# Performance work log

Measured on AMD Instinct MI355X. Metric: run time of the kernel, lower is better.

Reference implementation:

```python
import jax, jax.numpy as jnp
import numpy as np

K, N = 4, 128
NODEDIM = 256
EDGEDIM_IN = 256
EDGEDIM_OUT = 256
GLOBALDIM = 256
INFODIM = 2 * NODEDIM + GLOBALDIM + EDGEDIM_IN  # 1024


def setup_inputs() -> dict:
    key = jax.random.key(0)
    ks = jax.random.split(key, 10)
    u = jax.random.normal(ks[0], (K, GLOBALDIM), dtype=jnp.float32)
    h_v = jax.random.normal(ks[1], (K, N, NODEDIM), dtype=jnp.float32)
    h_e = jax.random.normal(ks[2], (K, N, N, EDGEDIM_IN), dtype=jnp.float32)
    V = jax.random.randint(ks[3], (K, N), 0, 2).astype(jnp.float32)  # binary node mask
    E = jax.random.randint(ks[4], (K, N, N, 2), 0, 2, dtype=jnp.int32)  # per-type edge mask
    # function[1] params (loop runs i in [1, num_functions) -> only i=1)
    s1 = 1.0 / np.sqrt(INFODIM)
    W1 = jax.random.uniform(ks[5], (INFODIM, INFODIM), jnp.float32, -s1, s1)
    b1 = jax.random.uniform(ks[6], (INFODIM,), jnp.float32, -s1, s1)
    W2 = jax.random.uniform(ks[7], (INFODIM, EDGEDIM_OUT), jnp.float32, -s1, s1)
    b2 = jax.random.uniform(ks[8], (EDGEDIM_OUT,), jnp.float32, -s1, s1)
    return {"u": u, "h_v": h_v, "h_e": h_e, "V": V, "E": E,
            "W1": W1, "b1": b1, "W2": W2, "b2": b2}


def reference(u, h_v, h_e, V, E, W1, b1, W2, b2):
    Kb, Nn = h_v.shape[0], h_v.shape[1]
    hv = h_v * V[..., None]                                    # masked node states
    src = jnp.broadcast_to(hv[:, :, None, :], (Kb, Nn, Nn, NODEDIM))
    tgt = jnp.broadcast_to(hv[:, None, :, :], (Kb, Nn, Nn, NODEDIM))
    glb = jnp.broadcast_to(u[:, None, None, :], (Kb, Nn, Nn, GLOBALDIM))
    edge_feat = jnp.concatenate([src, tgt, glb, h_e], axis=-1)  # [K,N,N,INFODIM]
    # per-type MLP (only function index 1 executes for num_functions=2)
    h = jax.nn.elu(jnp.einsum('knmi,ij->knmj', edge_feat, W1) + b1)
    out = jnp.einsum('knmi,io->knmo', h, W2) + b2               # [K,N,N,EDGEDIM_OUT]
    mask = (E[..., 1] == 1)[..., None]
    h_e_update = jnp.where(mask, out, jnp.zeros((), out.dtype))
    # residual=True, history=True
    return h_e_update + h_e
```

## Files before the change

kernel.cpp:

```cpp
#include <hip/hip_runtime.h>
#include <stdint.h>

#define DEVI __device__ __forceinline__

typedef short bf16x8 __attribute__((ext_vector_type(8)));
typedef float f32x4  __attribute__((ext_vector_type(4)));

DEVI short f2bf(float f){
  union { float f; uint32_t u; } un; un.f = f;
  uint32_t u = un.u;
  u += 0x7fffu + ((u >> 16) & 1u);
  return (short)(u >> 16);
}
DEVI float bf2f(uint32_t us){
  union { uint32_t u; float f; } x; x.u = us << 16; return x.f;
}

DEVI f32x4 mfma16(bf16x8 a, bf16x8 b, f32x4 c){
  return __builtin_amdgcn_mfma_f32_16x16x32_bf16(a, b, c, 0, 0, 0);
}

__global__ void transpose_bf(const float* __restrict__ W, short* __restrict__ WT,
                             int R, int C){
  __shared__ float tile[32][33];
  int ctiles = C >> 5;
  int bi = blockIdx.x / ctiles, bj = blockIdx.x % ctiles;
  int tx = threadIdx.x & 31, ty = threadIdx.x >> 5;
  #pragma unroll
  for (int r = 0; r < 4; ++r){
    int i = bi*32 + ty + r*8;
    tile[ty + r*8][tx] = W[(size_t)i*C + bj*32 + tx];
  }
  __syncthreads();
  #pragma unroll
  for (int r = 0; r < 4; ++r){
    int j = bj*32 + ty + r*8;
    WT[(size_t)j*R + bi*32 + tx] = f2bf(tile[tx][ty + r*8]);
  }
}

__global__ void prep_hv(const float* __restrict__ hv, const float* __restrict__ V,
                        const float* __restrict__ u, short* __restrict__ hvb,
                        short* __restrict__ ub){
  int idx = blockIdx.x*256 + threadIdx.x;
  if (idx < 512*256){
    int r = idx >> 8;
    hvb[idx] = f2bf(hv[idx] * V[r]);
  } else if (idx < 512*256 + 1024){
    int i2 = idx - 512*256;
    ub[i2] = f2bf(u[i2]);
  }
}

__global__ __launch_bounds__(256) void prep_st(
    const short* __restrict__ hvb, const short* __restrict__ ub,
    const short* __restrict__ w1t, const float* __restrict__ b1,
    short* __restrict__ sbuf, short* __restrict__ tbuf)
{
  const int bid = blockIdx.x;
  const int st = bid >> 7;
  const int rt8 = (bid >> 4) & 7;
  const int ctile = bid & 15;
  const int r0 = rt8 << 6, j0 = ctile << 6;
  const int tid = threadIdx.x;
  const int w = tid >> 6, l = tid & 63;
  const int l15 = l & 15, l4 = l >> 4;
  __shared__ short A[64*256];
  for (int q = 0; q < 8; ++q){
    int id = tid + (q << 8);
    int row = id >> 5, c8 = id & 31;
    bf16x8 v = *(const bf16x8*)(hvb + (size_t)(r0 + row)*256 + c8*8);
    *(bf16x8*)((char*)A + row*512 + ((c8*16) ^ ((row & 7) << 4))) = v;
  }
  __syncthreads();
  const int wr = w >> 1, wc = w & 1;
  const int rowbase = wr << 5, colbase = wc << 5;
  const int swzA = (l15 & 7) << 4;
  f32x4 acc[2][2];
  acc[0][0]=0; acc[0][1]=0; acc[1][0]=0; acc[1][1]=0;
  const int ioff = st ? 256 : 0;
  const short* w1p = w1t + (size_t)(j0 + colbase + l15)*1024 + ioff + l4*8;
  const char* ap0 = (const char*)A + (rowbase + l15)*512;
  const char* ap1 = ap0 + 16*512;
  #pragma unroll
  for (int kk = 0; kk < 8; ++kk){
    int ib = kk*64 + l4*16;
    bf16x8 a0 = *(const bf16x8*)(ap0 + (ib ^ swzA));
    bf16x8 a1 = *(const bf16x8*)(ap1 + (ib ^ swzA));
    bf16x8 b0 = *(const bf16x8*)(w1p + kk*32);
    bf16x8 b1v = *(const bf16x8*)(w1p + 16*1024 + kk*32);
    acc[0][0] = mfma16(a0, b0, acc[0][0]);
    acc[1][0] = mfma16(a1, b0, acc[1][0]);
    acc[0][1] = mfma16(a0, b1v, acc[0][1]);
    acc[1][1] = mfma16(a1, b1v, acc[1][1]);
  }
  if (st == 0){
    const int kb = r0 >> 7;
    const short* up = ub + kb*256 + l4*8;
    const short* w1pu = w1t + (size_t)(j0 + colbase + l15)*1024 + 512 + l4*8;
    #pragma unroll
    for (int kk = 0; kk < 8; ++kk){
      bf16x8 au = *(const bf16x8*)(up + kk*32);
      bf16x8 b0 = *(const bf16x8*)(w1pu + kk*32);
      bf16x8 b1v = *(const bf16x8*)(w1pu + 16*1024 + kk*32);
      acc[0][0] = mfma16(au, b0, acc[0][0]);
      acc[1][0] = mfma16(au, b0, acc[1][0]);
      acc[0][1] = mfma16(au, b1v, acc[0][1]);
      acc[1][1] = mfma16(au, b1v, acc[1][1]);
    }
  }
  #pragma unroll
  for (int r = 0; r < 2; ++r){
    #pragma unroll
    for (int c = 0; c < 2; ++c){
      int jg = j0 + colbase + c*16 + l15;
      float badd = st ? 0.f : b1[jg];
      #pragma unroll
      for (int reg = 0; reg < 4; ++reg){
        int rowl = rowbase + r*16 + l4*4 + reg;
        if (st == 0)
          sbuf[(size_t)(r0 + rowl)*1024 + jg] = f2bf(acc[r][c][reg] + badd);
        else
          tbuf[(size_t)jg*512 + (r0 + rowl)] = f2bf(acc[r][c][reg]);
      }
    }
  }
}

__global__ __launch_bounds__(256, 3) void fused_edge(
    const float* __restrict__ he, const unsigned short* __restrict__ sb,
    const unsigned short* __restrict__ tbT, const short* __restrict__ w1t,
    const short* __restrict__ w2t, const float* __restrict__ b2,
    const int* __restrict__ Em, float* __restrict__ out)
{
  const int b = blockIdx.x;
  const int k = b >> 8;
  const int n = (b >> 1) & 127;
  const int m0 = (b & 1) << 6;
  const int tid = threadIdx.x;
  const int w = tid >> 6, l = tid & 63;
  const int l15 = l & 15, l4 = l >> 4;

  __shared__ short heb[64*256];
  __shared__ short eluv[2][64*64];

  const int grow0 = ((k << 7) + n)*128 + m0;
  const float* hesrc = he + (size_t)grow0 * 256;

  #pragma unroll
  for (int q = 0; q < 8; ++q){
    int id = tid + (q << 8);
    int row = id >> 5, c8 = id & 31;
    const float4* p = (const float4*)(hesrc + row*256 + c8*8);
    float4 a4 = p[0], b4 = p[1];
    union { bf16x8 v; short s[8]; } pk;
    pk.s[0]=f2bf(a4.x); pk.s[1]=f2bf(a4.y); pk.s[2]=f2bf(a4.z); pk.s[3]=f2bf(a4.w);
    pk.s[4]=f2bf(b4.x); pk.s[5]=f2bf(b4.y); pk.s[6]=f2bf(b4.z); pk.s[7]=f2bf(b4.w);
    *(bf16x8*)((char*)heb + row*512 + ((c8*16) ^ ((row & 7) << 4))) = pk.v;
  }
  __syncthreads();

  f32x4 acc2[4][4];
  #pragma unroll
  for (int i = 0; i < 4; ++i)
    #pragma unroll
    for (int j = 0; j < 4; ++j) acc2[i][j] = 0;

  const unsigned short* srow = sb  + (size_t)((k << 7) + n)*1024;
  const unsigned short* tcol = tbT + (size_t)((k << 7) + m0);
  const char* hb = (const char*)heb;
  const int swz = (l15 & 7) << 4;

  union u4 { ushort4 v; unsigned short s[4]; };

  bf16x8 bw1[8];
  {
    const short* w1p = w1t + (size_t)(w*16 + l15)*1024 + 768 + l4*8;
    #pragma unroll
    for (int kk = 0; kk < 8; ++kk) bw1[kk] = *(const bf16x8*)(w1p + kk*32);
  }
  u4 t4[4];
  #pragma unroll
  for (int rt = 0; rt < 4; ++rt)
    t4[rt].v = *(const ushort4*)(tcol + (size_t)(w*16 + l15)*512 + rt*16 + l4*4);
  float sv = bf2f(srow[w*16 + l15]);

  #pragma unroll
  for (int jc = 0; jc < 16; ++jc){
    const int jcol = jc*64 + w*16 + l15;

    f32x4 acc1[4];
    acc1[0]=0; acc1[1]=0; acc1[2]=0; acc1[3]=0;
    #pragma unroll
    for (int kk = 0; kk < 8; ++kk){
      int ib = kk*64 + l4*16;
      #pragma unroll
      for (int rt = 0; rt < 4; ++rt){
        int row = rt*16 + l15;
        bf16x8 a = *(const bf16x8*)(hb + row*512 + (ib ^ swz));
        acc1[rt] = mfma16(a, bw1[kk], acc1[rt]);
      }
    }

    const short* w2p = w2t + (size_t)(w*64 + l15)*1024 + jc*64 + l4*8;
    bf16x8 bw2a[4];
    #pragma unroll
    for (int q = 0; q < 4; ++q)
      bw2a[q] = *(const bf16x8*)(w2p + (size_t)q*16*1024);

    if (jc < 15){
      const short* w1p = w1t + (size_t)(jcol + 64)*1024 + 768 + l4*8;
      #pragma unroll
      for (int kk = 0; kk < 8; ++kk) bw1[kk] = *(const bf16x8*)(w1p + kk*32);
    }

    char* eb = (char*)eluv[jc & 1];
    #pragma unroll
    for (int rt = 0; rt < 4; ++rt){
      #pragma unroll
      for (int reg = 0; reg < 4; ++reg){
        int row = rt*16 + l4*4 + reg;
        float v = acc1[rt][reg] + sv + bf2f(t4[rt].s[reg]);
        v = v > 0.f ? v : (__expf(v) - 1.f);
        *(short*)(eb + row*128 + ((((w*16 + l15)*2)) ^ ((row & 7) << 4))) = f2bf(v);
      }
    }

    if (jc < 15){
      #pragma unroll
      for (int rt = 0; rt < 4; ++rt)
        t4[rt].v = *(const ushort4*)(tcol + (size_t)(jcol + 64)*512 + rt*16 + l4*4);
      sv = bf2f(srow[jcol + 64]);
    }
    __syncthreads();

    bf16x8 bw2b[4];
    #pragma unroll
    for (int q = 0; q < 4; ++q)
      bw2b[q] = *(const bf16x8*)(w2p + (size_t)q*16*1024 + 32);

    {
      int jb = l4*16;
      #pragma unroll
      for (int rt = 0; rt < 4; ++rt){
        int row = rt*16 + l15;
        bf16x8 a2 = *(const bf16x8*)(eb + row*128 + (jb ^ swz));
        #pragma unroll
        for (int q = 0; q < 4; ++q)
          acc2[rt][q] = mfma16(a2, bw2a[q], acc2[rt][q]);
      }
      jb = 64 + l4*16;
      #pragma unroll
      for (int rt = 0; rt < 4; ++rt){
        int row = rt*16 + l15;
        bf16x8 a2 = *(const bf16x8*)(eb + row*128 + (jb ^ swz));
        #pragma unroll
        for (int q = 0; q < 4; ++q)
          acc2[rt][q] = mfma16(a2, bw2b[q], acc2[rt][q]);
      }
    }
  }

  float bias[4];
  #pragma unroll
  for (int q = 0; q < 4; ++q) bias[q] = b2[w*64 + q*16 + l15];
  #pragma unroll
  for (int rt = 0; rt < 4; ++rt){
    #pragma unroll
    for (int reg = 0; reg < 4; ++reg){
      int row = rt*16 + l4*4 + reg;
      size_t grow = (size_t)(grow0 + row);
      int2 ep = *(const int2*)(Em + grow*2);
      const float* hep = he + grow*256 + w*64 + l15;
      float* op = out + grow*256 + w*64 + l15;
      #pragma unroll
      for (int q = 0; q < 4; ++q){
        float v = (ep.y == 1) ? (acc2[rt][q][reg] + bias[q]) : 0.f;
        op[q*16] = v + hep[q*16];
      }
    }
  }
}

extern "C" void kernel_launch(void* const* d_in, const int* in_sizes, int n_in,
                              void* d_out, int out_size, void* d_ws, size_t ws_size,
                              hipStream_t stream)
{
  const float* u   = (const float*)d_in[0];
  const float* h_v = (const float*)d_in[1];
  const float* h_e = (const float*)d_in[2];
  const float* V   = (const float*)d_in[3];
  const int*   E   = (const int*)d_in[4];
  const float* W1  = (const float*)d_in[5];
  const float* b1  = (const float*)d_in[6];
  const float* W2  = (const float*)d_in[7];
  const float* b2  = (const float*)d_in[8];
  float* out = (float*)d_out;

  char* ws = (char*)d_ws;
  short* w1t  = (short*)(ws);
  short* w2t  = (short*)(ws + (2u<<20));
  short* hvb  = (short*)(ws + (2u<<20) + (512u<<10));
  short* ub   = (short*)(ws + (2u<<20) + (768u<<10));
  short* sbuf = (short*)(ws + (3u<<20));
  short* tbuf = (short*)(ws + (4u<<20));

  transpose_bf<<<1024, 256, 0, stream>>>(W1, w1t, 1024, 1024);
  transpose_bf<<<256,  256, 0, stream>>>(W2, w2t, 1024, 256);
  prep_hv<<<516, 256, 0, stream>>>(h_v, V, u, hvb, ub);
  prep_st<<<256, 256, 0, stream>>>(hvb, ub, w1t, b1, sbuf, tbuf);
  fused_edge<<<1024, 256, 0, stream>>>(h_e,
                                       (const unsigned short*)sbuf,
                                       (const unsigned short*)tbuf,
                                       w1t, w2t, b2, E, out);
}
```

Measured before the change: 201.8 us.

## Single-buffer ELU tile for higher occupancy, coalesce prep stores, nontemporal he traffic

The fused kernel drops the double-buffered ELU LDS tile in favour of one buffer with an extra barrier per column chunk. This cuts LDS per block so launch bounds can rise from 3 to 4 blocks per SIMD. The prep kernel now stages its output tile in shared memory and writes 16-byte coalesced rows instead of scattered 2-byte stores. h_e loads and output stores use nontemporal hints to avoid polluting cache. The extra barrier serialises the ELU write against the previous chunk's second GEMM, and the tighter launch bound may force register spills.

```diff
diff --git a/kernel.cpp b/kernel.cpp
--- a/kernel.cpp
+++ b/kernel.cpp
@@ -66,6 +66,7 @@
   const int w = tid >> 6, l = tid & 63;
   const int l15 = l & 15, l4 = l >> 4;
   __shared__ short A[64*256];
+  __shared__ short Stile[64][64];
   for (int q = 0; q < 8; ++q){
     int id = tid + (q << 8);
     int row = id >> 5, c8 = id & 31;
@@ -113,21 +114,31 @@
   for (int r = 0; r < 2; ++r){
     #pragma unroll
     for (int c = 0; c < 2; ++c){
-      int jg = j0 + colbase + c*16 + l15;
-      float badd = st ? 0.f : b1[jg];
+      int jl = colbase + c*16 + l15;
+      float badd = st ? 0.f : b1[j0 + jl];
       #pragma unroll
       for (int reg = 0; reg < 4; ++reg){
         int rowl = rowbase + r*16 + l4*4 + reg;
-        if (st == 0)
-          sbuf[(size_t)(r0 + rowl)*1024 + jg] = f2bf(acc[r][c][reg] + badd);
-        else
-          tbuf[(size_t)jg*512 + (r0 + rowl)] = f2bf(acc[r][c][reg]);
-      }
-    }
-  }
-}
-
-__global__ __launch_bounds__(256, 3) void fused_edge(
+        short v = f2bf(acc[r][c][reg] + badd);
+        if (st == 0) Stile[rowl][jl] = v;
+        else         Stile[jl][rowl] = v;
+      }
+    }
+  }
+  __syncthreads();
+  {
+    int a = tid >> 2, ch = (tid & 3) << 4;
+    bf16x8 v0 = *(const bf16x8*)(&Stile[a][ch]);
+    bf16x8 v1 = *(const bf16x8*)(&Stile[a][ch + 8]);
+    short* dst = (st == 0)
+      ? (sbuf + (size_t)(r0 + a)*1024 + j0 + ch)
+      : (tbuf + (size_t)(j0 + a)*512  + r0 + ch);
+    *(bf16x8*)(dst)     = v0;
+    *(bf16x8*)(dst + 8) = v1;
+  }
+}
+
+__global__ __launch_bounds__(256, 4) void fused_edge(
     const float* __restrict__ he, const unsigned short* __restrict__ sb,
     const unsigned short* __restrict__ tbT, const short* __restrict__ w1t,
     const short* __restrict__ w2t, const float* __restrict__ b2,
@@ -142,7 +153,7 @@
   const int l15 = l & 15, l4 = l >> 4;
 
   __shared__ short heb[64*256];
-  __shared__ short eluv[2][64*64];
+  __shared__ short eluv[64*64];
 
   const int grow0 = ((k << 7) + n)*128 + m0;
   const float* hesrc = he + (size_t)grow0 * 256;
@@ -151,8 +162,9 @@
   for (int q = 0; q < 8; ++q){
     int id = tid + (q << 8);
     int row = id >> 5, c8 = id & 31;
-    const float4* p = (const float4*)(hesrc + row*256 + c8*8);
-    float4 a4 = p[0], b4 = p[1];
+    const f32x4* p = (const f32x4*)(hesrc + row*256 + c8*8);
+    f32x4 a4 = __builtin_nontemporal_load(p);
+    f32x4 b4 = __builtin_nontemporal_load(p + 1);
     union { bf16x8 v; short s[8]; } pk;
     pk.s[0]=f2bf(a4.x); pk.s[1]=f2bf(a4.y); pk.s[2]=f2bf(a4.z); pk.s[3]=f2bf(a4.w);
     pk.s[4]=f2bf(b4.x); pk.s[5]=f2bf(b4.y); pk.s[6]=f2bf(b4.z); pk.s[7]=f2bf(b4.w);
@@ -214,7 +226,9 @@
       for (int kk = 0; kk < 8; ++kk) bw1[kk] = *(const bf16x8*)(w1p + kk*32);
     }
 
-    char* eb = (char*)eluv[jc & 1];
+    __syncthreads();
+
+    char* eb = (char*)eluv;
     #pragma unroll
     for (int rt = 0; rt < 4; ++rt){
       #pragma unroll
@@ -275,8 +289,9 @@
       float* op = out + grow*256 + w*64 + l15;
       #pragma unroll
       for (int q = 0; q < 4; ++q){
+        float hv = __builtin_nontemporal_load(hep + q*16);
         float v = (ep.y == 1) ? (acc2[rt][q][reg] + bias[q]) : 0.f;
-        op[q*16] = v + hep[q*16];
+        __builtin_nontemporal_store(v + hv, op + q*16);
       }
     }
   }
```

Result: slower. 365.6 us (+81.2%).
